# Optimization experiments

Hardware: AMD Instinct MI355X
Metric: run time of the kernel (lower is better)

## Reference

```python
import jax, jax.numpy as jnp
import numpy as np


def setup_inputs() -> dict:
    key = jax.random.key(0)
    ks = jax.random.split(key, 8)
    B, L, DIM, INNER = 4, 4096, 1024, 512
    return {
        "x": jax.random.normal(ks[0], (B, L, DIM), dtype=jnp.float32),
        "w_a": jax.random.normal(ks[1], (2 * INNER, DIM), dtype=jnp.float32) * (DIM ** -0.5),
        "w_x": jax.random.normal(ks[2], (2 * INNER, DIM), dtype=jnp.float32) * (DIM ** -0.5),
        "w_out": jax.random.normal(ks[3], (DIM, INNER), dtype=jnp.float32) * (INNER ** -0.5),
        "mat_v_real": jax.random.normal(ks[4], (INNER, INNER), dtype=jnp.float32),
        "mat_v_imag": jax.random.normal(ks[5], (INNER, INNER), dtype=jnp.float32),
        "last_hidden_real": jax.random.normal(ks[6], (INNER,), dtype=jnp.float32),
        "last_hidden_imag": jax.random.normal(ks[7], (INNER,), dtype=jnp.float32),
    }


def reference(x, w_a, w_x, w_out, mat_v_real, mat_v_imag,
              last_hidden_real, last_hidden_imag):
    b, l, dim = x.shape
    inner = mat_v_real.shape[0]
    V = jax.lax.complex(mat_v_real, mat_v_imag)          # (inner, inner)
    Vinv = jnp.linalg.inv(V)
    h0 = jax.lax.complex(last_hidden_real, last_hidden_imag)  # (inner,)

    xf = x.astype(jnp.float32)
    # decay gate a: complex, |a| = sigmoid(log|a_raw|^2) < 1
    a2 = (xf @ w_a.T).reshape(b, l, inner, 2)
    a_mag2 = a2[..., 0] ** 2 + a2[..., 1] ** 2
    a = jax.lax.complex(a2[..., 0], a2[..., 1]) * (
        jax.lax.rsqrt(a_mag2) * jax.nn.sigmoid(jnp.log(a_mag2)))

    # input projection: x_c <- x_c * |x_c|  (rsqrt(m)*m == sqrt(m))
    x2 = (xf @ w_x.T).reshape(b, l, inner, 2)
    x_mag2 = x2[..., 0] ** 2 + x2[..., 1] ** 2
    xc = jax.lax.complex(x2[..., 0], x2[..., 1]) * (jax.lax.rsqrt(x_mag2) * x_mag2)

    # x_roll[t] = xc[t-1], x_roll[0] = last_hidden (broadcast over batch)
    x_roll = jnp.concatenate(
        [jnp.broadcast_to(h0, (b, 1, inner)), xc[:, :-1]], axis=1)

    # Original builds c[l,m] = prod_{k=l..m} a_k via FFT cumsum of logs, then
    # V diag(c) V^{-1} contracted with x_roll. Equivalent diagonal recurrence:
    #   u_t = V^{-1} x_roll_t ;  s_t = a_t * s_{t-1} + a_t * u_t ;  h_t = V s_t + xc_t
    u = jnp.einsum('mn,bln->blm', Vinv, x_roll)

    def combine(c1, c2):
        a1, b1 = c1
        a2_, b2 = c2
        return (a2_ * a1, a2_ * b1 + b2)

    _, s = jax.lax.associative_scan(combine, (a, a * u), axis=1)
    h = jnp.einsum('mn,bln->blm', V, s) + xc                 # (b, l, inner) complex
    return (h.real @ w_out.T).astype(x.dtype)                # (b, l, dim)
```

## Files before the change

### kernel.cpp

```cpp
#include <hip/hip_runtime.h>

typedef unsigned short u16;
typedef short bf16x8 __attribute__((ext_vector_type(8)));
typedef float f32x4 __attribute__((ext_vector_type(4)));

typedef const __attribute__((address_space(1))) void* gaddr_t;
typedef __attribute__((address_space(3))) void* laddr_t;

__device__ __forceinline__ u16 f2b(float f){
  unsigned u = __float_as_uint(f);
  u = (u + 0x7fffu + ((u >> 16) & 1u)) >> 16;
  return (u16)u;
}
__device__ __forceinline__ float b2f(u16 h){
  return __uint_as_float(((unsigned)h) << 16);
}
__device__ __forceinline__ float2 cmul(float2 a, float2 b){
  return make_float2(a.x*b.x - a.y*b.y, a.x*b.y + a.y*b.x);
}

__global__ void cast_all(const float* __restrict__ x, const float* __restrict__ wa,
                         const float* __restrict__ wx, const float* __restrict__ wo,
                         u16* __restrict__ Xb, u16* __restrict__ WABb,
                         u16* __restrict__ WOb){
  int i = blockIdx.x*blockDim.x + threadIdx.x;
  int st = gridDim.x*blockDim.x;
  for (int idx = i; idx < 4849664; idx += st){
    const float* s; u16* d; int o;
    if (idx < 4194304){ s = x; d = Xb; o = idx; }
    else if (idx < 4456448){ s = wa; d = WABb; o = idx - 4194304; }
    else if (idx < 4718592){ s = wx; d = WABb + 1048576; o = idx - 4456448; }
    else { s = wo; d = WOb; o = idx - 4718592; }
    float4 v = ((const float4*)s)[o];
    ushort4 r; r.x=f2b(v.x); r.y=f2b(v.y); r.z=f2b(v.z); r.w=f2b(v.w);
    ((ushort4*)d)[o] = r;
  }
}

__global__ void inv_init(const float* __restrict__ vr, const float* __restrict__ vi,
                         float2* __restrict__ aug, float2* __restrict__ prow){
  int idx = blockIdx.x*256 + threadIdx.x;
  int r = idx >> 10, c = idx & 1023;
  float2 v;
  if (c < 512) v = make_float2(vr[r*512+c], vi[r*512+c]);
  else         v = make_float2((c-512)==r ? 1.f : 0.f, 0.f);
  aug[idx] = v;
  if (r < 32 && c >= 32) prow[idx] = v;
}

__device__ __forceinline__ void gj32(float2 (&L)[32][33], float2 (&R)[32][33],
                                     float2* fcol, int tid){
  for (int k = 0; k < 32; ++k){
    if (tid < 64){
      int lane = tid;
      float2 colv = make_float2(0.f, 0.f);
      float mag = -1.f;
      if (lane < 32){
        colv = L[lane][k];
        if (lane >= k) mag = colv.x*colv.x + colv.y*colv.y;
      }
      int best = lane;
      #pragma unroll
      for (int off = 1; off < 32; off <<= 1){
        float om = __shfl_xor(mag, off);
        int ob  = __shfl_xor(best, off);
        if (om > mag || (om == mag && ob < best)){ mag = om; best = ob; }
      }
      int p = __shfl(best, 0);
      float pvx = __shfl(colv.x, p), pvy = __shfl(colv.y, p);
      float dinv = 1.f / (pvx*pvx + pvy*pvy);
      float2 pinv = make_float2(pvx*dinv, -pvy*dinv);
      float2 rk = (lane < 32) ? L[k][lane] : R[k][lane-32];
      float2 rp = (lane < 32) ? L[p][lane] : R[p][lane-32];
      float2 nk = cmul(rp, pinv);
      if (lane < 32) L[k][lane] = nk; else R[k][lane-32] = nk;
      if (p != k){ if (lane < 32) L[p][lane] = rk; else R[p][lane-32] = rk; }
      if (lane < 32){
        float2 f = colv;
        float okx = __shfl(colv.x, k), oky = __shfl(colv.y, k);
        if (lane == p){ f.x = okx; f.y = oky; }
        fcol[lane] = f;
      }
    }
    __syncthreads();
    #pragma unroll
    for (int i = 0; i < 8; ++i){
      int idx = tid + i*256;
      int r = idx >> 6, c = idx & 63;
      if (r != k){
        float2 f = fcol[r];
        float2 nk = (c < 32) ? L[k][c] : R[k][c-32];
        float2 cell = (c < 32) ? L[r][c] : R[r][c-32];
        cell.x -= f.x*nk.x - f.y*nk.y;
        cell.y -= f.x*nk.y + f.y*nk.x;
        if (c < 32) L[r][c] = cell; else R[r][c-32] = cell;
      }
    }
    __syncthreads();
  }
}

__global__ __launch_bounds__(256) void inv_panel0(const float2* __restrict__ aug,
                                                  float2* __restrict__ binv){
  __shared__ float2 L[32][33];
  __shared__ float2 R[32][33];
  __shared__ float2 fcol[32];
  const int tid = threadIdx.x;
  for (int i = tid; i < 1024; i += 256){
    int r = i >> 5, c = i & 31;
    L[r][c] = aug[(size_t)r*1024 + c];
    R[r][c] = make_float2((r==c) ? 1.f : 0.f, 0.f);
  }
  __syncthreads();
  gj32(L, R, fcol, tid);
  for (int i = tid; i < 1024; i += 256) binv[i] = R[i>>5][i&31];
}

__global__ __launch_bounds__(256) void inv_update(float2* __restrict__ aug, int bs,
    const float2* __restrict__ prow, float2* __restrict__ prow_next,
    const float2* __restrict__ binv_in, float2* __restrict__ binv_out, int do_panel){
  __shared__ float2 Bi[32][33];
  __shared__ float2 Pr[32][33];
  __shared__ float2 T1[32][33];
  __shared__ float2 Pc[128][33];
  __shared__ float2 fcol[32];
  const int tid = threadIdx.x;
  const int c0 = bs + 32 + blockIdx.x*32;
  const int r0 = blockIdx.y*128;
  const bool panel = do_panel && (blockIdx.x == 0) && ((int)blockIdx.y == ((bs+32) >> 7));
  for (int idx = tid; idx < 1024; idx += 256){
    Bi[idx>>5][idx&31] = binv_in[idx];
    Pr[idx>>5][idx&31] = prow[(size_t)(idx>>5)*1024 + c0 + (idx&31)];
  }
  for (int idx = tid; idx < 128*32; idx += 256){
    int rr = idx>>5, j = idx&31;
    Pc[rr][j] = aug[(size_t)(r0+rr)*1024 + bs + j];
  }
  __syncthreads();
  for (int idx = tid; idx < 1024; idx += 256){
    int j = idx>>5, cc2 = idx&31;
    float2 acc = make_float2(0.f, 0.f);
    #pragma unroll
    for (int kk = 0; kk < 32; ++kk){
      float2 bv = Bi[j][kk], sv = Pr[kk][cc2];
      acc.x += bv.x*sv.x - bv.y*sv.y;
      acc.y += bv.x*sv.y + bv.y*sv.x;
    }
    T1[j][cc2] = acc;
  }
  __syncthreads();
  const int cc = tid & 31;
  float2 t1c[32];
  #pragma unroll
  for (int j = 0; j < 32; ++j) t1c[j] = T1[j][cc];
  __syncthreads();
  #pragma unroll 4
  for (int i = 0; i < 16; ++i){
    int idx = tid + i*256;
    int rr = idx>>5;
    int r = r0+rr, c = c0+cc;
    float2 nv;
    if (r >= bs && r < bs+32){
      nv = T1[r-bs][cc];
    } else {
      nv = aug[(size_t)r*1024 + c];
      #pragma unroll
      for (int j = 0; j < 32; ++j){
        float2 pq = Pc[rr][j], t = t1c[j];
        nv.x -= pq.x*t.x - pq.y*t.y;
        nv.y -= pq.x*t.y + pq.y*t.x;
      }
    }
    aug[(size_t)r*1024 + c] = nv;
    int rn = r - (bs+32);
    if (rn >= 0 && rn < 32){
      prow_next[(size_t)rn*1024 + c] = nv;
      if (panel) Bi[rn][cc] = nv;
    }
  }
  if (panel){
    __syncthreads();
    for (int i = tid; i < 1024; i += 256){
      int r = i>>5, c = i&31;
      Pr[r][c] = make_float2((r==c) ? 1.f : 0.f, 0.f);
    }
    __syncthreads();
    gj32(Bi, Pr, fcol, tid);
    for (int i = tid; i < 1024; i += 256) binv_out[i] = Pr[i>>5][i&31];
  }
}

__global__ void build_minv(const float2* __restrict__ aug, u16* __restrict__ Mi){
  int idx = blockIdx.x*256 + threadIdx.x;
  int row = idx >> 10, col = idx & 1023;
  int m = row >> 1, irow = row & 1;
  int k = col & 511, icol = col >> 9;
  float2 a = aug[(size_t)m*1024 + 512 + k];
  float v;
  if (!irow) v = icol ? -a.y : a.x;
  else       v = icol ?  a.x : a.y;
  Mi[idx] = f2b(v);
}
__global__ void build_mv4(const float* __restrict__ vr, const float* __restrict__ vi,
                          u16* __restrict__ Mv){
  int idx = blockIdx.x*256 + threadIdx.x;
  int m = idx >> 10, col = idx & 1023;
  int n = col >> 1;
  float v = (col & 1) ? -vi[m*512+n] : vr[m*512+n];
  Mv[idx] = f2b(v);
}
__global__ void fill_h0(const float* __restrict__ lhr, const float* __restrict__ lhi,
                        u16* __restrict__ xroll){
  int idx = blockIdx.x*256 + threadIdx.x;
  int b = idx >> 10, c = idx & 1023;
  float v = (c < 512) ? lhr[c] : lhi[c-512];
  xroll[(size_t)b*4096*1024 + c] = f2b(v);
}

enum { EPI_BF16 = 0, EPI_ADDXC = 3, EPI_OUTF32 = 4, EPI_AX = 5 };

#define MFMA_BF16(a,b,c) __builtin_amdgcn_mfma_f32_16x16x32_bf16(a,b,c,0,0,0)

template<int EPI>
__global__ __launch_bounds__(512, 2) void gemm256(
    const u16* __restrict__ A, const u16* __restrict__ B,
    int K, int NT, int N, int byShift,
    void* __restrict__ C, void* __restrict__ aux0, void* __restrict__ aux1,
    void* __restrict__ aux2)
{
  extern __shared__ u16 LDS[];
  const int tid = threadIdx.x;
  const int w = tid >> 6, lane = tid & 63;
  const int wm = w >> 2, wn = w & 3;
  const int fr = lane & 15, kg = lane >> 4;

  const int cpx = gridDim.x >> 3;
  const int bid = blockIdx.x;
  const int swz = (bid & 7)*cpx + (bid >> 3);
  const int by = swz & ((1 << byShift) - 1), bx = swz >> byShift;
  const size_t arow0 = (size_t)bx * 256;
  const int bcol0 = by * 256;

  const int rL = w*16 + (lane >> 2);
  const int glog = (lane & 3) ^ ((lane >> 3) & 3);
  const u16* Asrc = A + (arow0 + rL)*(size_t)K + glog*8;
  const u16* Bsrc = B + ((size_t)(bcol0 + rL))*K + glog*8;
  const size_t KH = (size_t)128 * K;
  const int sdst = w*512;

  const int goff = (kg ^ ((fr >> 1) & 3)) * 8;
  const int aro = wm*4096 + fr*32 + goff;
  const int bro = 32768 + (wn>>1)*4096 + (wn&1)*2048 + fr*32 + goff;

  f32x4 acc[8][4] = {};
  bf16x8 bfr[4];

  auto STG_A = [&](int kt){
    int bo = (kt & 3)*8192;
    #pragma unroll
    for (int h = 0; h < 2; ++h)
      __builtin_amdgcn_global_load_lds((gaddr_t)(Asrc + h*KH + kt*32),
          (laddr_t)(LDS + bo + h*4096 + sdst), 16, 0, 0);
  };
  auto STG_B = [&](int kt){
    int bo = 32768 + (kt & 3)*8192;
    #pragma unroll
    for (int h = 0; h < 2; ++h)
      __builtin_amdgcn_global_load_lds((gaddr_t)(Bsrc + h*KH + kt*32),
          (laddr_t)(LDS + bo + h*4096 + sdst), 16, 0, 0);
  };

  auto TILE = [&](int kt, int stg, int wait){
    const int ab = (kt & 3)*8192 + aro;
    const int bb = (kt & 3)*8192 + bro;
    bf16x8 af[4];
    #pragma unroll
    for (int m = 0; m < 4; ++m) af[m] = *(const bf16x8*)&LDS[ab + m*512];
    #pragma unroll
    for (int n = 0; n < 4; ++n) bfr[n] = *(const bf16x8*)&LDS[bb + n*512];
    if (stg) STG_A(kt + 3);
    __builtin_amdgcn_s_barrier();
    __builtin_amdgcn_s_setprio(1);
    #pragma unroll
    for (int m = 0; m < 4; ++m)
      #pragma unroll
      for (int n = 0; n < 4; ++n)
        acc[m][n] = MFMA_BF16(af[m], bfr[n], acc[m][n]);
    __builtin_amdgcn_s_setprio(0);
    __builtin_amdgcn_s_barrier();
    #pragma unroll
    for (int m = 0; m < 4; ++m) af[m] = *(const bf16x8*)&LDS[ab + (m+4)*512];
    if (stg) STG_B(kt + 3);
    __builtin_amdgcn_s_barrier();
    __builtin_amdgcn_s_setprio(1);
    #pragma unroll
    for (int m = 0; m < 4; ++m)
      #pragma unroll
      for (int n = 0; n < 4; ++n)
        acc[m+4][n] = MFMA_BF16(af[m], bfr[n], acc[m+4][n]);
    __builtin_amdgcn_s_setprio(0);
    if (wait == 2){ asm volatile("s_waitcnt vmcnt(8)" ::: "memory"); }
    else if (wait == 1){ asm volatile("s_waitcnt vmcnt(4)" ::: "memory"); }
    else if (wait == 0){ asm volatile("s_waitcnt vmcnt(0)" ::: "memory"); }
    __builtin_amdgcn_sched_barrier(0);
    __builtin_amdgcn_s_barrier();
  };

  STG_A(0); STG_B(0); STG_A(1); STG_B(1); STG_A(2); STG_B(2);
  asm volatile("s_waitcnt vmcnt(8)" ::: "memory");
  __builtin_amdgcn_sched_barrier(0);
  __builtin_amdgcn_s_barrier();

  #pragma unroll 1
  for (int kt = 0; kt < NT - 3; ++kt) TILE(kt, 1, 2);
  TILE(NT-3, 0, 1);
  TILE(NT-2, 0, 0);
  TILE(NT-1, 0, -1);

  const int rbase = wm*128 + (lane >> 4)*4;
  const int cbase = wn*64 + fr;
  #pragma unroll
  for (int M = 0; M < 8; ++M){
    #pragma unroll
    for (int Np = 0; Np < 4; ++Np){
      #pragma unroll
      for (int j = 0; j < 4; ++j){
        float v = acc[M][Np][j];
        size_t gr = arow0 + rbase + M*16 + j;
        int gc = bcol0 + cbase + Np*16;
        if constexpr (EPI == EPI_BF16){
          ((u16*)C)[gr*(size_t)N + gc] = f2b(v);
        } else if constexpr (EPI == EPI_OUTF32){
          ((float*)C)[gr*(size_t)N + gc] = v;
        } else if constexpr (EPI == EPI_ADDXC){
          float xc = b2f(((const u16*)aux0)[gr*512 + gc]);
          ((u16*)C)[gr*512 + gc] = f2b(v + xc);
        } else {
          float pv = __shfl_xor(v, 1);
          int odd = lane & 1;
          float re = odd ? pv : v;
          float im = odd ? v : pv;
          float m2 = re*re + im*im;
          if (gc < 1024){
            int mh = gc >> 1;
            float sc = m2 > 0.f ? sqrtf(m2)/(1.f + m2) : 0.f;
            if (!odd){
              unsigned pk = (unsigned)f2b(re*sc) | ((unsigned)f2b(im*sc) << 16);
              ((unsigned*)aux0)[gr*512 + mh] = pk;
            }
          } else {
            int mh = (gc - 1024) >> 1;
            float sc = sqrtf(m2);
            u16 ob = f2b(v * sc);
            if (!odd) ((u16*)aux1)[gr*512 + mh] = ob;
            int t = (int)(gr & 4095);
            if (t != 4095)
              ((u16*)aux2)[(gr+1)*1024 + (odd ? 512 + mh : mh)] = ob;
          }
        }
      }
    }
  }
}

__global__ void scan_p1(const unsigned* __restrict__ aint, const unsigned* __restrict__ uint_,
                        float4* __restrict__ agg){
  int idx = blockIdx.x*256 + threadIdx.x;
  int m = idx & 511, chunk = (idx >> 9) & 63, b = idx >> 15;
  size_t row = (size_t)b*4096 + chunk*64;
  float px=1.f, py=0.f, sx=0.f, sy=0.f;
  for (int i = 0; i < 64; ++i, ++row){
    unsigned av = aint[row*512 + m];
    unsigned uv = uint_[row*512 + m];
    float ar = b2f((u16)av), ai = b2f((u16)(av>>16));
    float ur = b2f((u16)uv), ui = b2f((u16)(uv>>16));
    float tx2 = sx + ur, ty2 = sy + ui;
    sx = ar*tx2 - ai*ty2; sy = ar*ty2 + ai*tx2;
    float np = px*ar - py*ai; py = px*ai + py*ar; px = np;
  }
  agg[((size_t)(b*512+m))*64 + chunk] = make_float4(px,py,sx,sy);
}
__global__ void scan_p2(const float4* __restrict__ agg, float2* __restrict__ carry){
  int seq = blockIdx.x*256 + threadIdx.x;
  float sx = 0.f, sy = 0.f;
  for (int c = 0; c < 64; ++c){
    carry[(size_t)seq*64 + c] = make_float2(sx, sy);
    float4 g = agg[(size_t)seq*64 + c];
    float nx = g.x*sx - g.y*sy + g.z;
    sy = g.x*sy + g.y*sx + g.w; sx = nx;
  }
}
__global__ void scan_p3(const unsigned* __restrict__ aint, const unsigned* __restrict__ uint_,
                        const float2* __restrict__ carry, unsigned* __restrict__ sout){
  int idx = blockIdx.x*256 + threadIdx.x;
  int m = idx & 511, chunk = (idx >> 9) & 63, b = idx >> 15;
  size_t row = (size_t)b*4096 + chunk*64;
  float2 c0 = carry[((size_t)(b*512+m))*64 + chunk];
  float sx = c0.x, sy = c0.y;
  for (int i = 0; i < 64; ++i, ++row){
    unsigned av = aint[row*512 + m];
    unsigned uv = uint_[row*512 + m];
    float ar = b2f((u16)av), ai = b2f((u16)(av>>16));
    float ur = b2f((u16)uv), ui = b2f((u16)(uv>>16));
    float tx2 = sx + ur, ty2 = sy + ui;
    sx = ar*tx2 - ai*ty2; sy = ar*ty2 + ai*tx2;
    sout[row*512 + m] = (unsigned)f2b(sx) | ((unsigned)f2b(sy) << 16);
  }
}

extern "C" void kernel_launch(void* const* d_in, const int* in_sizes, int n_in,
                              void* d_out, int out_size, void* d_ws, size_t ws_size,
                              hipStream_t stream){
  (void)in_sizes; (void)n_in; (void)out_size; (void)ws_size;
  const float* x   = (const float*)d_in[0];
  const float* wa  = (const float*)d_in[1];
  const float* wx  = (const float*)d_in[2];
  const float* wo  = (const float*)d_in[3];
  const float* vr  = (const float*)d_in[4];
  const float* vi  = (const float*)d_in[5];
  const float* lhr = (const float*)d_in[6];
  const float* lhi = (const float*)d_in[7];

  char* ws = (char*)d_ws;
  const size_t SB = 16384ull*1024*2;
  const size_t HB = SB/2;
  u16* Xb    = (u16*)(ws);
  unsigned* AINT = (unsigned*)(ws + SB);
  u16* XROLL = (u16*)(ws + 2*SB);
  u16* XCRE  = (u16*)(ws + 3*SB);
  char* p = ws + 3*SB + HB;
  u16* WABb  = (u16*)p; p += 4194304;
  u16* MINV  = (u16*)p; p += 2097152;
  u16* MV4   = (u16*)p; p += 1048576;
  u16* WOUTb = (u16*)p; p += 1048576;
  float2* AUG   = (float2*)p; p += 4194304;
  float2* PROWA = (float2*)p; p += 262144;
  float2* PROWB = (float2*)p; p += 262144;
  float2* BINV0 = (float2*)p; p += 8192;
  float2* BINV1 = (float2*)p; p += 8192;
  float4* AGG   = (float4*)p; p += 2048ull*64*16;
  float2* CARRY = (float2*)p; p += 2048ull*64*8;
  u16* U   = Xb;
  u16* S   = XROLL;
  u16* HRE = (u16*)AINT;

  cast_all<<<2048,256,0,stream>>>(x, wa, wx, wo, Xb, WABb, WOUTb);

  inv_init<<<2048,256,0,stream>>>(vr, vi, AUG, PROWA);
  inv_panel0<<<1,256,0,stream>>>(AUG, BINV0);
  float2* pr = PROWA; float2* prn = PROWB;
  for (int bs = 0; bs < 512; bs += 32){
    int step = bs >> 5;
    float2* bin  = (step & 1) ? BINV1 : BINV0;
    float2* bout = (step & 1) ? BINV0 : BINV1;
    inv_update<<<dim3((992-bs)/32, 4),256,0,stream>>>(AUG, bs, pr, prn, bin, bout,
                                                      bs < 480 ? 1 : 0);
    float2* t = pr; pr = prn; prn = t;
  }
  build_minv<<<4096,256,0,stream>>>(AUG, MINV);
  build_mv4<<<2048,256,0,stream>>>(vr, vi, MV4);
  fill_h0<<<16,256,0,stream>>>(lhr, lhi, XROLL);

  const size_t GLDS = 131072;
  gemm256<EPI_AX><<<512,512,GLDS,stream>>>(Xb, WABb, 1024, 32, 2048, 3,
                                           nullptr, (void*)AINT, (void*)XCRE, (void*)XROLL);
  gemm256<EPI_BF16><<<256,512,GLDS,stream>>>(XROLL, MINV, 1024, 32, 1024, 2,
                                             (void*)U, nullptr, nullptr, nullptr);

  scan_p1<<<512,256,0,stream>>>((const unsigned*)AINT, (const unsigned*)U, AGG);
  scan_p2<<<8,256,0,stream>>>(AGG, CARRY);
  scan_p3<<<512,256,0,stream>>>((const unsigned*)AINT, (const unsigned*)U, CARRY, (unsigned*)S);

  gemm256<EPI_ADDXC><<<128,512,GLDS,stream>>>(S, MV4, 1024, 32, 512, 1,
                                              (void*)HRE, (void*)XCRE, nullptr, nullptr);
  gemm256<EPI_OUTF32><<<256,512,GLDS,stream>>>(HRE, WOUTb, 512, 16, 1024, 2,
                                               d_out, nullptr, nullptr, nullptr);
}
```

Before: 1.300 ms.

## Fuse matrix-inverse launches into one persistent kernel with grid barriers

Replaces the chain of roughly twenty small inverse kernels (init, first panel, sixteen block-update steps, final Minv build) with one persistent kernel of 64 blocks. The blocks sync through an atomic grid barrier and loop over the update tasks that used to be separate grid blocks. The MV4 build and h0 fill are folded into the cast kernel, which removes more launches. This trades per-launch overhead for a spin barrier and fewer blocks per step. Only 64 blocks now share up to 124 tasks, and the code relies on all 64 blocks being co-resident.

```diff
diff --git a/kernel.cpp b/kernel.cpp
--- a/kernel.cpp
+++ b/kernel.cpp
@@ -6,6 +6,8 @@
 
 typedef const __attribute__((address_space(1))) void* gaddr_t;
 typedef __attribute__((address_space(3))) void* laddr_t;
+
+#define NB_INV 64
 
 __device__ __forceinline__ u16 f2b(float f){
   unsigned u = __float_as_uint(f);
@@ -21,31 +23,38 @@
 
 __global__ void cast_all(const float* __restrict__ x, const float* __restrict__ wa,
                          const float* __restrict__ wx, const float* __restrict__ wo,
+                         const float* __restrict__ vr, const float* __restrict__ vi,
+                         const float* __restrict__ lhr, const float* __restrict__ lhi,
                          u16* __restrict__ Xb, u16* __restrict__ WABb,
-                         u16* __restrict__ WOb){
+                         u16* __restrict__ WOb, u16* __restrict__ Mv,
+                         u16* __restrict__ xroll){
   int i = blockIdx.x*blockDim.x + threadIdx.x;
   int st = gridDim.x*blockDim.x;
-  for (int idx = i; idx < 4849664; idx += st){
-    const float* s; u16* d; int o;
-    if (idx < 4194304){ s = x; d = Xb; o = idx; }
-    else if (idx < 4456448){ s = wa; d = WABb; o = idx - 4194304; }
-    else if (idx < 4718592){ s = wx; d = WABb + 1048576; o = idx - 4456448; }
-    else { s = wo; d = WOb; o = idx - 4718592; }
-    float4 v = ((const float4*)s)[o];
-    ushort4 r; r.x=f2b(v.x); r.y=f2b(v.y); r.z=f2b(v.z); r.w=f2b(v.w);
-    ((ushort4*)d)[o] = r;
-  }
-}
-
-__global__ void inv_init(const float* __restrict__ vr, const float* __restrict__ vi,
-                         float2* __restrict__ aug, float2* __restrict__ prow){
-  int idx = blockIdx.x*256 + threadIdx.x;
-  int r = idx >> 10, c = idx & 1023;
-  float2 v;
-  if (c < 512) v = make_float2(vr[r*512+c], vi[r*512+c]);
-  else         v = make_float2((c-512)==r ? 1.f : 0.f, 0.f);
-  aug[idx] = v;
-  if (r < 32 && c >= 32) prow[idx] = v;
+  for (int idx = i; idx < 4981760; idx += st){
+    if (idx < 4849664){
+      const float* s; u16* d; int o;
+      if (idx < 4194304){ s = x; d = Xb; o = idx; }
+      else if (idx < 4456448){ s = wa; d = WABb; o = idx - 4194304; }
+      else if (idx < 4718592){ s = wx; d = WABb + 1048576; o = idx - 4456448; }
+      else { s = wo; d = WOb; o = idx - 4718592; }
+      float4 v = ((const float4*)s)[o];
+      ushort4 r; r.x=f2b(v.x); r.y=f2b(v.y); r.z=f2b(v.z); r.w=f2b(v.w);
+      ((ushort4*)d)[o] = r;
+    } else if (idx < 4980736){
+      int o = idx - 4849664;
+      int m = o >> 8, q = o & 255;
+      float2 a = ((const float2*)vr)[m*256 + q];
+      float2 b = ((const float2*)vi)[m*256 + q];
+      ushort4 r; r.x=f2b(a.x); r.y=f2b(-b.x); r.z=f2b(a.y); r.w=f2b(-b.y);
+      ((ushort4*)Mv)[o] = r;
+    } else {
+      int o = idx - 4980736;
+      int b = o >> 8, c4 = o & 255;
+      float4 v = (c4 < 128) ? ((const float4*)lhr)[c4] : ((const float4*)lhi)[c4-128];
+      ushort4 r; r.x=f2b(v.x); r.y=f2b(v.y); r.z=f2b(v.z); r.w=f2b(v.w);
+      ((ushort4*)xroll)[b*1048576 + c4] = r;
+    }
+  }
 }
 
 __device__ __forceinline__ void gj32(float2 (&L)[32][33], float2 (&R)[32][33],
@@ -100,121 +109,142 @@
   }
 }
 
-__global__ __launch_bounds__(256) void inv_panel0(const float2* __restrict__ aug,
-                                                  float2* __restrict__ binv){
-  __shared__ float2 L[32][33];
-  __shared__ float2 R[32][33];
-  __shared__ float2 fcol[32];
-  const int tid = threadIdx.x;
-  for (int i = tid; i < 1024; i += 256){
-    int r = i >> 5, c = i & 31;
-    L[r][c] = aug[(size_t)r*1024 + c];
-    R[r][c] = make_float2((r==c) ? 1.f : 0.f, 0.f);
-  }
-  __syncthreads();
-  gj32(L, R, fcol, tid);
-  for (int i = tid; i < 1024; i += 256) binv[i] = R[i>>5][i&31];
-}
-
-__global__ __launch_bounds__(256) void inv_update(float2* __restrict__ aug, int bs,
-    const float2* __restrict__ prow, float2* __restrict__ prow_next,
-    const float2* __restrict__ binv_in, float2* __restrict__ binv_out, int do_panel){
+__global__ __launch_bounds__(256) void inv_persist(
+    const float* __restrict__ vr, const float* __restrict__ vi,
+    float2* __restrict__ aug, float2* __restrict__ prA, float2* __restrict__ prB,
+    float2* __restrict__ bv0, float2* __restrict__ bv1,
+    u16* __restrict__ Mi, int* __restrict__ bar)
+{
   __shared__ float2 Bi[32][33];
   __shared__ float2 Pr[32][33];
   __shared__ float2 T1[32][33];
+  __shared__ float2 Nd[32][33];
   __shared__ float2 Pc[128][33];
   __shared__ float2 fcol[32];
-  const int tid = threadIdx.x;
-  const int c0 = bs + 32 + blockIdx.x*32;
-  const int r0 = blockIdx.y*128;
-  const bool panel = do_panel && (blockIdx.x == 0) && ((int)blockIdx.y == ((bs+32) >> 7));
-  for (int idx = tid; idx < 1024; idx += 256){
-    Bi[idx>>5][idx&31] = binv_in[idx];
-    Pr[idx>>5][idx&31] = prow[(size_t)(idx>>5)*1024 + c0 + (idx&31)];
-  }
-  for (int idx = tid; idx < 128*32; idx += 256){
-    int rr = idx>>5, j = idx&31;
-    Pc[rr][j] = aug[(size_t)(r0+rr)*1024 + bs + j];
-  }
-  __syncthreads();
-  for (int idx = tid; idx < 1024; idx += 256){
-    int j = idx>>5, cc2 = idx&31;
-    float2 acc = make_float2(0.f, 0.f);
-    #pragma unroll
-    for (int kk = 0; kk < 32; ++kk){
-      float2 bv = Bi[j][kk], sv = Pr[kk][cc2];
-      acc.x += bv.x*sv.x - bv.y*sv.y;
-      acc.y += bv.x*sv.y + bv.y*sv.x;
-    }
-    T1[j][cc2] = acc;
-  }
-  __syncthreads();
-  const int cc = tid & 31;
-  float2 t1c[32];
-  #pragma unroll
-  for (int j = 0; j < 32; ++j) t1c[j] = T1[j][cc];
-  __syncthreads();
-  #pragma unroll 4
-  for (int i = 0; i < 16; ++i){
-    int idx = tid + i*256;
-    int rr = idx>>5;
-    int r = r0+rr, c = c0+cc;
-    float2 nv;
-    if (r >= bs && r < bs+32){
-      nv = T1[r-bs][cc];
-    } else {
-      nv = aug[(size_t)r*1024 + c];
-      #pragma unroll
-      for (int j = 0; j < 32; ++j){
-        float2 pq = Pc[rr][j], t = t1c[j];
-        nv.x -= pq.x*t.x - pq.y*t.y;
-        nv.y -= pq.x*t.y + pq.y*t.x;
-      }
-    }
-    aug[(size_t)r*1024 + c] = nv;
-    int rn = r - (bs+32);
-    if (rn >= 0 && rn < 32){
-      prow_next[(size_t)rn*1024 + c] = nv;
-      if (panel) Bi[rn][cc] = nv;
-    }
-  }
-  if (panel){
+  const int tid = threadIdx.x, blk = blockIdx.x;
+  int nbar = 0;
+
+  auto GBAR = [&](){
     __syncthreads();
+    __threadfence();
+    if (tid == 0){
+      ++nbar;
+      __hip_atomic_fetch_add(bar, 1, __ATOMIC_ACQ_REL, __HIP_MEMORY_SCOPE_AGENT);
+      while (__hip_atomic_load(bar, __ATOMIC_ACQUIRE, __HIP_MEMORY_SCOPE_AGENT) < nbar*NB_INV)
+        __builtin_amdgcn_s_sleep(2);
+    }
+    __syncthreads();
+    __threadfence();
+  };
+
+  for (int i = blk*256 + tid; i < 512*1024; i += NB_INV*256){
+    int r = i >> 10, c = i & 1023;
+    float2 v = (c < 512) ? make_float2(vr[r*512+c], vi[r*512+c])
+                         : make_float2((c-512)==r ? 1.f : 0.f, 0.f);
+    aug[i] = v;
+    if (r < 32) prA[(size_t)r*1024 + c] = v;
+  }
+  GBAR();
+
+  if (blk == 0){
     for (int i = tid; i < 1024; i += 256){
       int r = i>>5, c = i&31;
+      Nd[r][c] = aug[(size_t)r*1024 + c];
       Pr[r][c] = make_float2((r==c) ? 1.f : 0.f, 0.f);
     }
     __syncthreads();
-    gj32(Bi, Pr, fcol, tid);
-    for (int i = tid; i < 1024; i += 256) binv_out[i] = Pr[i>>5][i&31];
-  }
-}
-
-__global__ void build_minv(const float2* __restrict__ aug, u16* __restrict__ Mi){
-  int idx = blockIdx.x*256 + threadIdx.x;
-  int row = idx >> 10, col = idx & 1023;
-  int m = row >> 1, irow = row & 1;
-  int k = col & 511, icol = col >> 9;
-  float2 a = aug[(size_t)m*1024 + 512 + k];
-  float v;
-  if (!irow) v = icol ? -a.y : a.x;
-  else       v = icol ?  a.x : a.y;
-  Mi[idx] = f2b(v);
-}
-__global__ void build_mv4(const float* __restrict__ vr, const float* __restrict__ vi,
-                          u16* __restrict__ Mv){
-  int idx = blockIdx.x*256 + threadIdx.x;
-  int m = idx >> 10, col = idx & 1023;
-  int n = col >> 1;
-  float v = (col & 1) ? -vi[m*512+n] : vr[m*512+n];
-  Mv[idx] = f2b(v);
-}
-__global__ void fill_h0(const float* __restrict__ lhr, const float* __restrict__ lhi,
-                        u16* __restrict__ xroll){
-  int idx = blockIdx.x*256 + threadIdx.x;
-  int b = idx >> 10, c = idx & 1023;
-  float v = (c < 512) ? lhr[c] : lhi[c-512];
-  xroll[(size_t)b*4096*1024 + c] = f2b(v);
+    gj32(Nd, Pr, fcol, tid);
+    for (int i = tid; i < 1024; i += 256) bv0[i] = Pr[i>>5][i&31];
+  }
+  GBAR();
+
+  for (int step = 0; step < 16; ++step){
+    const int bs = step*32;
+    float2* bin   = (step&1) ? bv1 : bv0;
+    float2* bout  = (step&1) ? bv0 : bv1;
+    float2* prin  = (step&1) ? prB : prA;
+    float2* prout = (step&1) ? prA : prB;
+    for (int i = tid; i < 1024; i += 256) Bi[i>>5][i&31] = bin[i];
+    const int ncs = (992 - bs) >> 5;
+    const int ntask = ncs*4;
+    const int prg = (bs + 32) >> 7;
+    bool havePanel = false;
+    for (int t = blk; t < ntask; t += NB_INV){
+      const int strip = t >> 2, rg = t & 3;
+      const int c0 = bs + 32 + strip*32;
+      const int r0 = rg*128;
+      const bool panel = (step < 15) && (strip == 0) && (rg == prg);
+      __syncthreads();
+      for (int i = tid; i < 1024; i += 256)
+        Pr[i>>5][i&31] = prin[(size_t)(i>>5)*1024 + c0 + (i&31)];
+      for (int i = tid; i < 4096; i += 256)
+        Pc[i>>5][i&31] = aug[(size_t)(r0 + (i>>5))*1024 + bs + (i&31)];
+      __syncthreads();
+      for (int i = tid; i < 1024; i += 256){
+        int j = i>>5, cc2 = i&31;
+        float2 acc = make_float2(0.f, 0.f);
+        #pragma unroll
+        for (int kk = 0; kk < 32; ++kk){
+          float2 bv = Bi[j][kk], sv = Pr[kk][cc2];
+          acc.x += bv.x*sv.x - bv.y*sv.y;
+          acc.y += bv.x*sv.y + bv.y*sv.x;
+        }
+        T1[j][cc2] = acc;
+      }
+      __syncthreads();
+      const int cc = tid & 31;
+      float2 t1c[32];
+      #pragma unroll
+      for (int j = 0; j < 32; ++j) t1c[j] = T1[j][cc];
+      #pragma unroll 4
+      for (int i = 0; i < 16; ++i){
+        int idx = tid + i*256;
+        int rr = idx >> 5;
+        int r = r0 + rr, c = c0 + cc;
+        float2 nv;
+        if (r >= bs && r < bs+32){
+          nv = T1[r-bs][cc];
+        } else {
+          nv = aug[(size_t)r*1024 + c];
+          #pragma unroll
+          for (int j = 0; j < 32; ++j){
+            float2 pq = Pc[rr][j], tt = t1c[j];
+            nv.x -= pq.x*tt.x - pq.y*tt.y;
+            nv.y -= pq.x*tt.y + pq.y*tt.x;
+          }
+        }
+        aug[(size_t)r*1024 + c] = nv;
+        int rn = r - (bs+32);
+        if (rn >= 0 && rn < 32){
+          prout[(size_t)rn*1024 + c] = nv;
+          if (panel) Nd[rn][cc] = nv;
+        }
+      }
+      if (panel) havePanel = true;
+    }
+    if (havePanel){
+      __syncthreads();
+      for (int i = tid; i < 1024; i += 256){
+        int r = i>>5, c = i&31;
+        Pr[r][c] = make_float2((r==c) ? 1.f : 0.f, 0.f);
+      }
+      __syncthreads();
+      gj32(Nd, Pr, fcol, tid);
+      for (int i = tid; i < 1024; i += 256) bout[i] = Pr[i>>5][i&31];
+    }
+    GBAR();
+  }
+
+  for (int i = blk*256 + tid; i < 1048576; i += NB_INV*256){
+    int row = i >> 10, col = i & 1023;
+    int m = row >> 1, irow = row & 1;
+    int k = col & 511, icol = col >> 9;
+    float2 a = aug[(size_t)m*1024 + 512 + k];
+    float v;
+    if (!irow) v = icol ? -a.y : a.x;
+    else       v = icol ?  a.x : a.y;
+    Mi[i] = f2b(v);
+  }
 }
 
 enum { EPI_BF16 = 0, EPI_ADDXC = 3, EPI_OUTF32 = 4, EPI_AX = 5 };
@@ -440,26 +470,18 @@
   float2* BINV1 = (float2*)p; p += 8192;
   float4* AGG   = (float4*)p; p += 2048ull*64*16;
   float2* CARRY = (float2*)p; p += 2048ull*64*8;
+  int*    BAR   = (int*)p;   p += 256;
   u16* U   = Xb;
   u16* S   = XROLL;
   u16* HRE = (u16*)AINT;
 
-  cast_all<<<2048,256,0,stream>>>(x, wa, wx, wo, Xb, WABb, WOUTb);
-
-  inv_init<<<2048,256,0,stream>>>(vr, vi, AUG, PROWA);
-  inv_panel0<<<1,256,0,stream>>>(AUG, BINV0);
-  float2* pr = PROWA; float2* prn = PROWB;
-  for (int bs = 0; bs < 512; bs += 32){
-    int step = bs >> 5;
-    float2* bin  = (step & 1) ? BINV1 : BINV0;
-    float2* bout = (step & 1) ? BINV0 : BINV1;
-    inv_update<<<dim3((992-bs)/32, 4),256,0,stream>>>(AUG, bs, pr, prn, bin, bout,
-                                                      bs < 480 ? 1 : 0);
-    float2* t = pr; pr = prn; prn = t;
-  }
-  build_minv<<<4096,256,0,stream>>>(AUG, MINV);
-  build_mv4<<<2048,256,0,stream>>>(vr, vi, MV4);
-  fill_h0<<<16,256,0,stream>>>(lhr, lhi, XROLL);
+  hipMemsetAsync(BAR, 0, 256, stream);
+
+  cast_all<<<2048,256,0,stream>>>(x, wa, wx, wo, vr, vi, lhr, lhi,
+                                  Xb, WABb, WOUTb, MV4, XROLL);
+
+  inv_persist<<<NB_INV,256,0,stream>>>(vr, vi, AUG, PROWA, PROWB, BINV0, BINV1,
+                                       MINV, BAR);
 
   const size_t GLDS = 131072;
   gemm256<EPI_AX><<<512,512,GLDS,stream>>>(Xb, WABb, 1024, 32, 2048, 3,
```

Result: slower. 1.950 ms (+50.0%).

## Use 64-wide blocked Gauss-Jordan inverse and fold small prep kernels into cast

Applied to the files above, without the earlier changes.

Reworks the matrix inversion from 16 steps with a 32-wide panel into 8 steps with a 64-wide panel. Each block now redundantly inverts the diagonal 64x64 panel itself, which removes the separate panel kernel and the hand-off of the panel inverse between launches. The V-matrix bf16 build and the h0 fill are folded into the cast kernel, so several launches go away. In exchange every block repeats the serial 64-step pivot elimination and needs about 134KB of LDS, which limits occupancy on the update.

```diff
diff --git a/kernel.cpp b/kernel.cpp
--- a/kernel.cpp
+++ b/kernel.cpp
@@ -21,19 +21,37 @@
 
 __global__ void cast_all(const float* __restrict__ x, const float* __restrict__ wa,
                          const float* __restrict__ wx, const float* __restrict__ wo,
+                         const float* __restrict__ vr, const float* __restrict__ vi,
+                         const float* __restrict__ lhr, const float* __restrict__ lhi,
                          u16* __restrict__ Xb, u16* __restrict__ WABb,
-                         u16* __restrict__ WOb){
+                         u16* __restrict__ WOb, u16* __restrict__ Mv,
+                         u16* __restrict__ xroll){
   int i = blockIdx.x*blockDim.x + threadIdx.x;
   int st = gridDim.x*blockDim.x;
-  for (int idx = i; idx < 4849664; idx += st){
-    const float* s; u16* d; int o;
-    if (idx < 4194304){ s = x; d = Xb; o = idx; }
-    else if (idx < 4456448){ s = wa; d = WABb; o = idx - 4194304; }
-    else if (idx < 4718592){ s = wx; d = WABb + 1048576; o = idx - 4456448; }
-    else { s = wo; d = WOb; o = idx - 4718592; }
-    float4 v = ((const float4*)s)[o];
-    ushort4 r; r.x=f2b(v.x); r.y=f2b(v.y); r.z=f2b(v.z); r.w=f2b(v.w);
-    ((ushort4*)d)[o] = r;
+  for (int idx = i; idx < 4981760; idx += st){
+    if (idx < 4849664){
+      const float* s; u16* d; int o;
+      if (idx < 4194304){ s = x; d = Xb; o = idx; }
+      else if (idx < 4456448){ s = wa; d = WABb; o = idx - 4194304; }
+      else if (idx < 4718592){ s = wx; d = WABb + 1048576; o = idx - 4456448; }
+      else { s = wo; d = WOb; o = idx - 4718592; }
+      float4 v = ((const float4*)s)[o];
+      ushort4 r; r.x=f2b(v.x); r.y=f2b(v.y); r.z=f2b(v.z); r.w=f2b(v.w);
+      ((ushort4*)d)[o] = r;
+    } else if (idx < 4980736){
+      int o = idx - 4849664;
+      int m = o >> 8, q = o & 255;
+      float2 a = ((const float2*)vr)[m*256 + q];
+      float2 b = ((const float2*)vi)[m*256 + q];
+      ushort4 r; r.x=f2b(a.x); r.y=f2b(-b.x); r.z=f2b(a.y); r.w=f2b(-b.y);
+      ((ushort4*)Mv)[o] = r;
+    } else {
+      int o = idx - 4980736;
+      int b = o >> 8, c4 = o & 255;
+      float4 v = (c4 < 128) ? ((const float4*)lhr)[c4] : ((const float4*)lhi)[c4-128];
+      ushort4 r; r.x=f2b(v.x); r.y=f2b(v.y); r.z=f2b(v.z); r.w=f2b(v.w);
+      ((ushort4*)xroll)[b*1048576 + c4] = r;
+    }
   }
 }
 
@@ -45,148 +63,140 @@
   if (c < 512) v = make_float2(vr[r*512+c], vi[r*512+c]);
   else         v = make_float2((c-512)==r ? 1.f : 0.f, 0.f);
   aug[idx] = v;
-  if (r < 32 && c >= 32) prow[idx] = v;
-}
-
-__device__ __forceinline__ void gj32(float2 (&L)[32][33], float2 (&R)[32][33],
-                                     float2* fcol, int tid){
-  for (int k = 0; k < 32; ++k){
+  if (r < 64) prow[(size_t)r*1024 + c] = v;
+}
+
+__device__ __forceinline__ void gj64(float2* T, float2* fcol, float* ps, int tid){
+  const int LD = 129;
+  #pragma unroll 1
+  for (int k = 0; k < 64; ++k){
     if (tid < 64){
       int lane = tid;
-      float2 colv = make_float2(0.f, 0.f);
-      float mag = -1.f;
-      if (lane < 32){
-        colv = L[lane][k];
-        if (lane >= k) mag = colv.x*colv.x + colv.y*colv.y;
-      }
+      float2 colv = T[lane*LD + k];
+      float mag = (lane >= k) ? (colv.x*colv.x + colv.y*colv.y) : -1.f;
       int best = lane;
       #pragma unroll
-      for (int off = 1; off < 32; off <<= 1){
+      for (int off = 1; off < 64; off <<= 1){
         float om = __shfl_xor(mag, off);
         int ob  = __shfl_xor(best, off);
         if (om > mag || (om == mag && ob < best)){ mag = om; best = ob; }
       }
-      int p = __shfl(best, 0);
+      int p = best;
       float pvx = __shfl(colv.x, p), pvy = __shfl(colv.y, p);
-      float dinv = 1.f / (pvx*pvx + pvy*pvy);
-      float2 pinv = make_float2(pvx*dinv, -pvy*dinv);
-      float2 rk = (lane < 32) ? L[k][lane] : R[k][lane-32];
-      float2 rp = (lane < 32) ? L[p][lane] : R[p][lane-32];
-      float2 nk = cmul(rp, pinv);
-      if (lane < 32) L[k][lane] = nk; else R[k][lane-32] = nk;
-      if (p != k){ if (lane < 32) L[p][lane] = rk; else R[p][lane-32] = rk; }
-      if (lane < 32){
-        float2 f = colv;
-        float okx = __shfl(colv.x, k), oky = __shfl(colv.y, k);
-        if (lane == p){ f.x = okx; f.y = oky; }
-        fcol[lane] = f;
+      float okx = __shfl(colv.x, k), oky = __shfl(colv.y, k);
+      float dinv = 1.f/(pvx*pvx + pvy*pvy);
+      float2 f = colv;
+      if (lane == p){ f.x = okx; f.y = oky; }
+      fcol[lane] = f;
+      if (lane == 0){ ps[0] = pvx*dinv; ps[1] = -pvy*dinv; ps[2] = __int_as_float(p); }
+    }
+    __syncthreads();
+    {
+      int p = __float_as_int(ps[2]);
+      float2 pinv = make_float2(ps[0], ps[1]);
+      if (tid < 128){
+        int col = tid;
+        float2 rk = T[k*LD + col];
+        float2 rp = T[p*LD + col];
+        float2 nk = cmul(rp, pinv);
+        T[k*LD + col] = nk;
+        if (p != k) T[p*LD + col] = rk;
       }
     }
     __syncthreads();
     #pragma unroll
-    for (int i = 0; i < 8; ++i){
-      int idx = tid + i*256;
-      int r = idx >> 6, c = idx & 63;
+    for (int i = 0; i < 16; ++i){
+      int idx = tid + i*512;
+      int r = idx >> 7, c = idx & 127;
       if (r != k){
-        float2 f = fcol[r];
-        float2 nk = (c < 32) ? L[k][c] : R[k][c-32];
-        float2 cell = (c < 32) ? L[r][c] : R[r][c-32];
+        float2 f = fcol[r], nk = T[k*LD + c];
+        float2 cell = T[r*LD + c];
         cell.x -= f.x*nk.x - f.y*nk.y;
         cell.y -= f.x*nk.y + f.y*nk.x;
-        if (c < 32) L[r][c] = cell; else R[r][c-32] = cell;
+        T[r*LD + c] = cell;
       }
     }
     __syncthreads();
   }
 }
 
-__global__ __launch_bounds__(256) void inv_panel0(const float2* __restrict__ aug,
-                                                  float2* __restrict__ binv){
-  __shared__ float2 L[32][33];
-  __shared__ float2 R[32][33];
-  __shared__ float2 fcol[32];
+__global__ __launch_bounds__(512) void inv_step64(
+    float2* __restrict__ aug, int bs,
+    const float2* __restrict__ prin, float2* __restrict__ prout)
+{
+  extern __shared__ char lds[];
+  float2* U0   = (float2*)lds;
+  float2* Bi   = (float2*)(lds + 66560);
+  float2* Pr   = (float2*)(lds + 66560 + 33280);
+  float2* T1   = (float2*)(lds + 66560 + 33280 + 16896);
+  float2* fcol = (float2*)(lds + 66560 + 33280 + 33792);
+  float*  ps   = (float*) (lds + 66560 + 33280 + 33792 + 512);
+
   const int tid = threadIdx.x;
-  for (int i = tid; i < 1024; i += 256){
-    int r = i >> 5, c = i & 31;
-    L[r][c] = aug[(size_t)r*1024 + c];
-    R[r][c] = make_float2((r==c) ? 1.f : 0.f, 0.f);
+  const int c0 = bs + 64 + blockIdx.x*32;
+  const int r0 = blockIdx.y*128;
+
+  for (int i = tid; i < 4096; i += 512){
+    int r = i >> 6, c = i & 63;
+    U0[r*129 + c]      = aug[(size_t)(bs+r)*1024 + bs + c];
+    U0[r*129 + 64 + c] = make_float2((r==c) ? 1.f : 0.f, 0.f);
   }
   __syncthreads();
-  gj32(L, R, fcol, tid);
-  for (int i = tid; i < 1024; i += 256) binv[i] = R[i>>5][i&31];
-}
-
-__global__ __launch_bounds__(256) void inv_update(float2* __restrict__ aug, int bs,
-    const float2* __restrict__ prow, float2* __restrict__ prow_next,
-    const float2* __restrict__ binv_in, float2* __restrict__ binv_out, int do_panel){
-  __shared__ float2 Bi[32][33];
-  __shared__ float2 Pr[32][33];
-  __shared__ float2 T1[32][33];
-  __shared__ float2 Pc[128][33];
-  __shared__ float2 fcol[32];
-  const int tid = threadIdx.x;
-  const int c0 = bs + 32 + blockIdx.x*32;
-  const int r0 = blockIdx.y*128;
-  const bool panel = do_panel && (blockIdx.x == 0) && ((int)blockIdx.y == ((bs+32) >> 7));
-  for (int idx = tid; idx < 1024; idx += 256){
-    Bi[idx>>5][idx&31] = binv_in[idx];
-    Pr[idx>>5][idx&31] = prow[(size_t)(idx>>5)*1024 + c0 + (idx&31)];
-  }
-  for (int idx = tid; idx < 128*32; idx += 256){
-    int rr = idx>>5, j = idx&31;
-    Pc[rr][j] = aug[(size_t)(r0+rr)*1024 + bs + j];
-  }
+  gj64(U0, fcol, ps, tid);
+  for (int i = tid; i < 4096; i += 512)
+    Bi[(i>>6)*65 + (i&63)] = U0[(i>>6)*129 + 64 + (i&63)];
+  for (int i = tid; i < 2048; i += 512)
+    Pr[(i>>5)*33 + (i&31)] = prin[(size_t)(i>>5)*1024 + c0 + (i&31)];
   __syncthreads();
-  for (int idx = tid; idx < 1024; idx += 256){
-    int j = idx>>5, cc2 = idx&31;
+
+  for (int i = tid; i < 8192; i += 512)
+    U0[(i>>6)*65 + (i&63)] = aug[(size_t)(r0 + (i>>6))*1024 + bs + (i&63)];
+  for (int i = tid; i < 2048; i += 512){
+    int j = i >> 5, cc = i & 31;
     float2 acc = make_float2(0.f, 0.f);
     #pragma unroll
-    for (int kk = 0; kk < 32; ++kk){
-      float2 bv = Bi[j][kk], sv = Pr[kk][cc2];
+    for (int kk = 0; kk < 64; ++kk){
+      float2 bv = Bi[j*65 + kk], sv = Pr[kk*33 + cc];
       acc.x += bv.x*sv.x - bv.y*sv.y;
       acc.y += bv.x*sv.y + bv.y*sv.x;
     }
-    T1[j][cc2] = acc;
+    T1[j*33 + cc] = acc;
   }
   __syncthreads();
-  const int cc = tid & 31;
-  float2 t1c[32];
+
+  const int cc = tid & 31, rbase = tid >> 5;
+  float2 nv[8];
   #pragma unroll
-  for (int j = 0; j < 32; ++j) t1c[j] = T1[j][cc];
-  __syncthreads();
-  #pragma unroll 4
-  for (int i = 0; i < 16; ++i){
-    int idx = tid + i*256;
-    int rr = idx>>5;
-    int r = r0+rr, c = c0+cc;
-    float2 nv;
-    if (r >= bs && r < bs+32){
-      nv = T1[r-bs][cc];
-    } else {
-      nv = aug[(size_t)r*1024 + c];
+  for (int i = 0; i < 8; ++i){
+    int rr = rbase + i*16;
+    nv[i] = aug[(size_t)(r0+rr)*1024 + c0 + cc];
+  }
+  #pragma unroll
+  for (int h = 0; h < 2; ++h){
+    float2 t1c[32];
+    #pragma unroll
+    for (int kk = 0; kk < 32; ++kk) t1c[kk] = T1[(h*32+kk)*33 + cc];
+    #pragma unroll
+    for (int i = 0; i < 8; ++i){
+      int rr = rbase + i*16;
+      float2 v = nv[i];
       #pragma unroll
-      for (int j = 0; j < 32; ++j){
-        float2 pq = Pc[rr][j], t = t1c[j];
-        nv.x -= pq.x*t.x - pq.y*t.y;
-        nv.y -= pq.x*t.y + pq.y*t.x;
+      for (int kk = 0; kk < 32; ++kk){
+        float2 f = U0[rr*65 + h*32 + kk];
+        v.x -= f.x*t1c[kk].x - f.y*t1c[kk].y;
+        v.y -= f.x*t1c[kk].y + f.y*t1c[kk].x;
       }
-    }
-    aug[(size_t)r*1024 + c] = nv;
-    int rn = r - (bs+32);
-    if (rn >= 0 && rn < 32){
-      prow_next[(size_t)rn*1024 + c] = nv;
-      if (panel) Bi[rn][cc] = nv;
-    }
-  }
-  if (panel){
-    __syncthreads();
-    for (int i = tid; i < 1024; i += 256){
-      int r = i>>5, c = i&31;
-      Pr[r][c] = make_float2((r==c) ? 1.f : 0.f, 0.f);
-    }
-    __syncthreads();
-    gj32(Bi, Pr, fcol, tid);
-    for (int i = tid; i < 1024; i += 256) binv_out[i] = Pr[i>>5][i&31];
+      nv[i] = v;
+    }
+  }
+  #pragma unroll
+  for (int i = 0; i < 8; ++i){
+    int rr = rbase + i*16;
+    int r = r0 + rr;
+    float2 out = (r >= bs && r < bs+64) ? T1[(r-bs)*33 + cc] : nv[i];
+    aug[(size_t)r*1024 + c0 + cc] = out;
+    int rn = r - (bs + 64);
+    if (rn >= 0 && rn < 64) prout[(size_t)rn*1024 + c0 + cc] = out;
   }
 }
 
@@ -200,21 +210,6 @@
   if (!irow) v = icol ? -a.y : a.x;
   else       v = icol ?  a.x : a.y;
   Mi[idx] = f2b(v);
-}
-__global__ void build_mv4(const float* __restrict__ vr, const float* __restrict__ vi,
-                          u16* __restrict__ Mv){
-  int idx = blockIdx.x*256 + threadIdx.x;
-  int m = idx >> 10, col = idx & 1023;
-  int n = col >> 1;
-  float v = (col & 1) ? -vi[m*512+n] : vr[m*512+n];
-  Mv[idx] = f2b(v);
-}
-__global__ void fill_h0(const float* __restrict__ lhr, const float* __restrict__ lhi,
-                        u16* __restrict__ xroll){
-  int idx = blockIdx.x*256 + threadIdx.x;
-  int b = idx >> 10, c = idx & 1023;
-  float v = (c < 512) ? lhr[c] : lhi[c-512];
-  xroll[(size_t)b*4096*1024 + c] = f2b(v);
 }
 
 enum { EPI_BF16 = 0, EPI_ADDXC = 3, EPI_OUTF32 = 4, EPI_AX = 5 };
@@ -434,32 +429,26 @@
   u16* MV4   = (u16*)p; p += 1048576;
   u16* WOUTb = (u16*)p; p += 1048576;
   float2* AUG   = (float2*)p; p += 4194304;
-  float2* PROWA = (float2*)p; p += 262144;
-  float2* PROWB = (float2*)p; p += 262144;
-  float2* BINV0 = (float2*)p; p += 8192;
-  float2* BINV1 = (float2*)p; p += 8192;
-  float4* AGG   = (float4*)p; p += 2048ull*64*16;
-  float2* CARRY = (float2*)p; p += 2048ull*64*8;
+  float2* PROWA = (float2*)p; p += 524288;
+  float2* PROWB = (float2*)p; p += 524288;
+  float4* AGG   = (float4*)AUG;
+  float2* CARRY = (float2*)((char*)AUG + 2097152);
   u16* U   = Xb;
   u16* S   = XROLL;
   u16* HRE = (u16*)AINT;
 
-  cast_all<<<2048,256,0,stream>>>(x, wa, wx, wo, Xb, WABb, WOUTb);
+  cast_all<<<2048,256,0,stream>>>(x, wa, wx, wo, vr, vi, lhr, lhi,
+                                  Xb, WABb, WOUTb, MV4, XROLL);
 
   inv_init<<<2048,256,0,stream>>>(vr, vi, AUG, PROWA);
-  inv_panel0<<<1,256,0,stream>>>(AUG, BINV0);
-  float2* pr = PROWA; float2* prn = PROWB;
-  for (int bs = 0; bs < 512; bs += 32){
-    int step = bs >> 5;
-    float2* bin  = (step & 1) ? BINV1 : BINV0;
-    float2* bout = (step & 1) ? BINV0 : BINV1;
-    inv_update<<<dim3((992-bs)/32, 4),256,0,stream>>>(AUG, bs, pr, prn, bin, bout,
-                                                      bs < 480 ? 1 : 0);
-    float2* t = pr; pr = prn; prn = t;
+  const size_t SLDS = 134160;
+  for (int step = 0; step < 8; ++step){
+    int bs = step*64;
+    float2* prin  = (step & 1) ? PROWB : PROWA;
+    float2* prout = (step & 1) ? PROWA : PROWB;
+    inv_step64<<<dim3((960 - bs)/32, 4), 512, SLDS, stream>>>(AUG, bs, prin, prout);
   }
   build_minv<<<4096,256,0,stream>>>(AUG, MINV);
-  build_mv4<<<2048,256,0,stream>>>(vr, vi, MV4);
-  fill_h0<<<16,256,0,stream>>>(lhr, lhi, XROLL);
 
   const size_t GLDS = 131072;
   gemm256<EPI_AX><<<512,512,GLDS,stream>>>(Xb, WABb, 1024, 32, 2048, 3,
```

Result: slower. 2.916 ms (+124.2%).
